# Kernel optimization log

Hardware: AMD Instinct MI355X
Metric: run time of the kernel (lower is better)

## Reference

```python
import jax, jax.numpy as jnp
import numpy as np

B, L, D = 32, 128, 512

def setup_inputs() -> dict:
    key = jax.random.key(0)
    ks = jax.random.split(key, 10)
    s = 1.0 / np.sqrt(D)
    return {
        "current_sotw": jax.random.normal(ks[0], (B, L, D), jnp.float32),
        "new_obs": jax.random.normal(ks[1], (B, L, D), jnp.float32),
        "Wq": jax.random.uniform(ks[2], (D, D), jnp.float32, -s, s),   # linear_query weight
        "bq": jax.random.uniform(ks[3], (D,), jnp.float32, -s, s),     # linear_query bias
        "Wc": jax.random.uniform(ks[4], (D, D), jnp.float32, -s, s),   # linear_context (no bias)
        "v": jax.random.uniform(ks[5], (D,), jnp.float32, -s, s),      # v projection to scalar score
        "Wout": jax.random.uniform(ks[6], (2 * D, D), jnp.float32, -s, s),  # linear_out weight
        "bout": jax.random.uniform(ks[7], (D,), jnp.float32, -s, s),        # linear_out bias (mlp type)
        "mix": jax.random.uniform(ks[8], (1,), jnp.float32),           # mixing_proportion ~ U[0,1)
    }

def _global_attn_mlp(source, memory, Wq, bq, Wc, v, Wout, bout):
    # OpenNMT GlobalAttention, attn_type='mlp', attn_func='softmax'
    wq = jnp.einsum('btd,de->bte', source, Wq) + bq          # [B,T,D]
    uh = jnp.einsum('bsd,de->bse', memory, Wc)               # [B,S,D]
    # scores: v . tanh(wq + uh) over broadcast [B,T,S,D]
    scores = jnp.einsum('btsd,d->bts', jnp.tanh(wq[:, :, None, :] + uh[:, None, :, :]), v)
    align = jax.nn.softmax(scores, axis=-1)                  # [B,T,S]
    c = jnp.einsum('bts,bsd->btd', align, memory)            # context [B,T,D]
    attn_h = jnp.einsum('btd,de->bte', jnp.concatenate([c, source], axis=-1), Wout) + bout
    return attn_h  # [B,T,D] (the torch code transposes to [T,B,D] then back)

def reference(current_sotw, new_obs, Wq, bq, Wc, v, Wout, bout, mix):
    a1 = _global_attn_mlp(new_obs, current_sotw, Wq, bq, Wc, v, Wout, bout)
    a2 = _global_attn_mlp(current_sotw, new_obs, Wq, bq, Wc, v, Wout, bout)
    m = mix[0]
    return (1.0 - m) * a1 + m * a2
```

## Files before the change

kernel.cpp:

```cpp
#include <hip/hip_runtime.h>

#define DD 512
#define SS 128
#define TT4 4
#define SCH16 16
#define RW 520
#define C2F 2.8853900817779268f
#define L2EF 1.4426950408889634f

typedef __bf16 bf16x8 __attribute__((ext_vector_type(8)));
typedef float f32x4 __attribute__((ext_vector_type(4)));
typedef unsigned int uint32x4 __attribute__((ext_vector_type(4)));

__device__ __forceinline__ unsigned short f2bf(float f) {
    unsigned int u = __builtin_bit_cast(unsigned int, f);
    u += 0x7fffu + ((u >> 16) & 1u);
    return (unsigned short)(u >> 16);
}
__device__ __forceinline__ float bflo(unsigned int u) { return __builtin_bit_cast(float, u << 16); }
__device__ __forceinline__ float bfhi(unsigned int u) { return __builtin_bit_cast(float, u & 0xffff0000u); }

__global__ __launch_bounds__(256)
void cvt_dual(const float* __restrict__ a, const float* __restrict__ b,
              unsigned short* __restrict__ oa, unsigned short* __restrict__ ob, int n8)
{
    int i = blockIdx.x * 256 + threadIdx.x;
    const float* in; unsigned short* out; int k;
    if (i < n8) { in = a; out = oa; k = i; }
    else        { in = b; out = ob; k = i - n8; }
    const float4 x = ((const float4*)in)[2 * k];
    const float4 y = ((const float4*)in)[2 * k + 1];
    uint32x4 o;
    o[0] = (unsigned)f2bf(x.x) | ((unsigned)f2bf(x.y) << 16);
    o[1] = (unsigned)f2bf(x.z) | ((unsigned)f2bf(x.w) << 16);
    o[2] = (unsigned)f2bf(y.x) | ((unsigned)f2bf(y.y) << 16);
    o[3] = (unsigned)f2bf(y.z) | ((unsigned)f2bf(y.w) << 16);
    ((uint32x4*)out)[k] = o;
}

__global__ __launch_bounds__(256)
void transpose_all(const float* __restrict__ Wq, const float* __restrict__ Wc,
                   const float* __restrict__ Wout,
                   unsigned short* __restrict__ Wqct, unsigned short* __restrict__ Woutt)
{
    __shared__ float t[64][65];
    const int z = blockIdx.z;
    const float* in; unsigned short* out; int R, r0;
    if (z == 0)      { in = Wq;   out = Wqct;             R = 512;  r0 = blockIdx.y * 64; }
    else if (z == 1) { in = Wc;   out = Wqct + 512 * 512; R = 512;  r0 = blockIdx.y * 64; }
    else             { in = Wout; out = Woutt;            R = 1024; r0 = (z - 2) * 512 + blockIdx.y * 64; }
    const int c0 = blockIdx.x * 64;
    const int tid = threadIdx.x;
    const int lc = tid & 63, lr = tid >> 6;
    #pragma unroll
    for (int i = 0; i < 16; ++i) {
        int r = lr + i * 4;
        t[r][lc] = in[(size_t)(r0 + r) * 512 + c0 + lc];
    }
    __syncthreads();
    #pragma unroll
    for (int i = 0; i < 16; ++i) {
        int rr = lr + i * 4;
        out[(size_t)(c0 + rr) * R + r0 + lc] = f2bf(t[lc][rr]);
    }
}

__global__ __launch_bounds__(256)
void gemm_proj(const unsigned short* __restrict__ A0, const unsigned short* __restrict__ A1,
               const unsigned short* __restrict__ Bt, const float* __restrict__ bq,
               unsigned short* __restrict__ w0, unsigned short* __restrict__ u0,
               unsigned short* __restrict__ w1, unsigned short* __restrict__ u1)
{
    constexpr int K = 512, LDA = 72;
    __shared__ __align__(16) unsigned short As[128][LDA];
    __shared__ __align__(16) unsigned short Bs[64][LDA];

    const unsigned short* A = blockIdx.z ? A1 : A0;
    unsigned short* outW    = blockIdx.z ? w1 : w0;
    unsigned short* outU    = blockIdx.z ? u1 : u0;

    const int tid = threadIdx.x;
    const int n0 = blockIdx.x * 64, m0 = blockIdx.y * 128;
    const int lane = tid & 63, wid = tid >> 6;
    const int wr = wid >> 1, wc = wid & 1;
    const int lr = lane & 15, kb = lane >> 4;

    f32x4 acc[4][2] = {};
    uint32x4 ra[4], rb[2];

    auto LOADK = [&](int k0) {
        #pragma unroll
        for (int j = 0; j < 4; ++j) {
            int id = tid + 256 * j; int r = id >> 3, s = id & 7;
            ra[j] = *(const uint32x4*)&A[(size_t)(m0 + r) * K + k0 + s * 8];
        }
        #pragma unroll
        for (int j = 0; j < 2; ++j) {
            int id = tid + 256 * j; int r = id >> 3, s = id & 7;
            rb[j] = *(const uint32x4*)&Bt[(size_t)(n0 + r) * K + k0 + s * 8];
        }
    };

    LOADK(0);
    #pragma unroll 1
    for (int step = 0; step < K / 64; ++step) {
        __syncthreads();
        #pragma unroll
        for (int j = 0; j < 4; ++j) {
            int id = tid + 256 * j; int r = id >> 3, s = id & 7;
            *(uint32x4*)&As[r][s * 8] = ra[j];
        }
        #pragma unroll
        for (int j = 0; j < 2; ++j) {
            int id = tid + 256 * j; int r = id >> 3, s = id & 7;
            *(uint32x4*)&Bs[r][s * 8] = rb[j];
        }
        __syncthreads();
        if (step + 1 < K / 64) LOADK((step + 1) * 64);
        #pragma unroll
        for (int kk = 0; kk < 64; kk += 32) {
            bf16x8 b0 = __builtin_bit_cast(bf16x8, *(const uint32x4*)&Bs[wc * 32 + lr][kk + kb * 8]);
            bf16x8 b1 = __builtin_bit_cast(bf16x8, *(const uint32x4*)&Bs[wc * 32 + 16 + lr][kk + kb * 8]);
            #pragma unroll
            for (int mf = 0; mf < 4; ++mf) {
                bf16x8 a0 = __builtin_bit_cast(bf16x8, *(const uint32x4*)&As[wr * 64 + mf * 16 + lr][kk + kb * 8]);
                acc[mf][0] = __builtin_amdgcn_mfma_f32_16x16x32_bf16(a0, b0, acc[mf][0], 0, 0, 0);
                acc[mf][1] = __builtin_amdgcn_mfma_f32_16x16x32_bf16(a0, b1, acc[mf][1], 0, 0, 0);
            }
        }
    }

    #pragma unroll
    for (int nf = 0; nf < 2; ++nf) {
        const int col = n0 + wc * 32 + nf * 16 + lr;
        const float bv = (col < 512) ? bq[col] : 0.0f;
        #pragma unroll
        for (int mf = 0; mf < 4; ++mf) {
            const int row = m0 + wr * 64 + mf * 16 + kb * 4;
            #pragma unroll
            for (int r = 0; r < 4; ++r) {
                const float valf = acc[mf][nf][r];
                if (col < 512) outW[(size_t)(row + r) * 512 + col] = f2bf((valf + bv) * C2F);
                else           outU[(size_t)(row + r) * 512 + (col - 512)] = f2bf(valf);
            }
        }
    }
}

__global__ __launch_bounds__(256)
void gemm_final(const unsigned short* __restrict__ c1, const unsigned short* __restrict__ c2,
                const float* __restrict__ no, const float* __restrict__ cs,
                const float* __restrict__ mix, const unsigned short* __restrict__ Bt,
                const float* __restrict__ bout, float* __restrict__ out)
{
    constexpr int K = 1024, LDA = 72;
    __shared__ __align__(16) unsigned short As[128][LDA];
    __shared__ __align__(16) unsigned short Bs[64][LDA];

    const int tid = threadIdx.x;
    const int n0 = blockIdx.x * 64, m0 = blockIdx.y * 128;
    const int lane = tid & 63, wid = tid >> 6;
    const int wr = wid >> 1, wc = wid & 1;
    const int lr = lane & 15, kb = lane >> 4;
    const float mxv = mix[0], omv = 1.0f - mxv;

    f32x4 acc[4][2] = {};
    uint32x4 ra[4], rb[2];

    auto LOADK = [&](int k0) {
        #pragma unroll
        for (int j = 0; j < 4; ++j) {
            int id = tid + 256 * j; int r = id >> 3, s = id & 7;
            const size_t row = m0 + r;
            const int k = k0 + s * 8;
            uint32x4 o;
            if (k < 512) {
                const uint32x4 x1 = *(const uint32x4*)&c1[row * 512 + k];
                const uint32x4 x2 = *(const uint32x4*)&c2[row * 512 + k];
                #pragma unroll
                for (int q = 0; q < 4; ++q) {
                    float lo = omv * bflo(x1[q]) + mxv * bflo(x2[q]);
                    float hi = omv * bfhi(x1[q]) + mxv * bfhi(x2[q]);
                    o[q] = (unsigned)f2bf(lo) | ((unsigned)f2bf(hi) << 16);
                }
            } else {
                const float* n1 = &no[row * 512 + k - 512];
                const float* s1 = &cs[row * 512 + k - 512];
                const float4 a1 = *(const float4*)n1, a2 = *(const float4*)(n1 + 4);
                const float4 b1 = *(const float4*)s1, b2 = *(const float4*)(s1 + 4);
                o[0] = (unsigned)f2bf(omv * a1.x + mxv * b1.x) | ((unsigned)f2bf(omv * a1.y + mxv * b1.y) << 16);
                o[1] = (unsigned)f2bf(omv * a1.z + mxv * b1.z) | ((unsigned)f2bf(omv * a1.w + mxv * b1.w) << 16);
                o[2] = (unsigned)f2bf(omv * a2.x + mxv * b2.x) | ((unsigned)f2bf(omv * a2.y + mxv * b2.y) << 16);
                o[3] = (unsigned)f2bf(omv * a2.z + mxv * b2.z) | ((unsigned)f2bf(omv * a2.w + mxv * b2.w) << 16);
            }
            ra[j] = o;
        }
        #pragma unroll
        for (int j = 0; j < 2; ++j) {
            int id = tid + 256 * j; int r = id >> 3, s = id & 7;
            rb[j] = *(const uint32x4*)&Bt[(size_t)(n0 + r) * K + k0 + s * 8];
        }
    };

    LOADK(0);
    #pragma unroll 1
    for (int step = 0; step < K / 64; ++step) {
        __syncthreads();
        #pragma unroll
        for (int j = 0; j < 4; ++j) {
            int id = tid + 256 * j; int r = id >> 3, s = id & 7;
            *(uint32x4*)&As[r][s * 8] = ra[j];
        }
        #pragma unroll
        for (int j = 0; j < 2; ++j) {
            int id = tid + 256 * j; int r = id >> 3, s = id & 7;
            *(uint32x4*)&Bs[r][s * 8] = rb[j];
        }
        __syncthreads();
        if (step + 1 < K / 64) LOADK((step + 1) * 64);
        #pragma unroll
        for (int kk = 0; kk < 64; kk += 32) {
            bf16x8 b0 = __builtin_bit_cast(bf16x8, *(const uint32x4*)&Bs[wc * 32 + lr][kk + kb * 8]);
            bf16x8 b1 = __builtin_bit_cast(bf16x8, *(const uint32x4*)&Bs[wc * 32 + 16 + lr][kk + kb * 8]);
            #pragma unroll
            for (int mf = 0; mf < 4; ++mf) {
                bf16x8 a0 = __builtin_bit_cast(bf16x8, *(const uint32x4*)&As[wr * 64 + mf * 16 + lr][kk + kb * 8]);
                acc[mf][0] = __builtin_amdgcn_mfma_f32_16x16x32_bf16(a0, b0, acc[mf][0], 0, 0, 0);
                acc[mf][1] = __builtin_amdgcn_mfma_f32_16x16x32_bf16(a0, b1, acc[mf][1], 0, 0, 0);
            }
        }
    }

    #pragma unroll
    for (int nf = 0; nf < 2; ++nf) {
        const int col = n0 + wc * 32 + nf * 16 + lr;
        const float bv = bout[col];
        #pragma unroll
        for (int mf = 0; mf < 4; ++mf) {
            const int row = m0 + wr * 64 + mf * 16 + kb * 4;
            #pragma unroll
            for (int r = 0; r < 4; ++r)
                out[(size_t)(row + r) * 512 + col] = acc[mf][nf][r] + bv;
        }
    }
}

__global__ __launch_bounds__(512, 8)
void attn_fused(const unsigned short* __restrict__ wq,
                const unsigned short* __restrict__ uh,
                const float* __restrict__ v,
                const unsigned short* __restrict__ mem,
                unsigned short* __restrict__ c_out)
{
    __shared__ __align__(16) unsigned short s_wq[TT4 * RW];
    __shared__ __align__(16) unsigned short s_uh[SCH16 * RW];
    __shared__ __align__(16) unsigned short s_v2[DD];
    __shared__ float s_sc[TT4 * SS];

    const int b = blockIdx.y, t0 = blockIdx.x * TT4;
    const int tid = threadIdx.x;

    if (tid < 256) {
        const int row = tid >> 6, G = tid & 63;
        *(uint32x4*)&s_wq[row * RW + G * 8] =
            *(const uint32x4*)&wq[((size_t)b * SS + t0 + row) * DD + G * 8];
    } else if (tid < 320) {
        const int H = tid - 256;
        const float4 p = *(const float4*)&v[H * 8];
        const float4 q = *(const float4*)&v[H * 8 + 4];
        uint32x4 o;
        o[0] = (unsigned)f2bf(p.x * 2.f) | ((unsigned)f2bf(p.y * 2.f) << 16);
        o[1] = (unsigned)f2bf(p.z * 2.f) | ((unsigned)f2bf(p.w * 2.f) << 16);
        o[2] = (unsigned)f2bf(q.x * 2.f) | ((unsigned)f2bf(q.y * 2.f) << 16);
        o[3] = (unsigned)f2bf(q.z * 2.f) | ((unsigned)f2bf(q.w * 2.f) << 16);
        *(uint32x4*)&s_v2[H * 8] = o;
    }

    const int oct = tid & 7;
    const int sr  = (tid >> 3) & 15;
    const int t   = tid >> 7;

    for (int sc0 = 0; sc0 < SS; sc0 += SCH16) {
        __syncthreads();
        {
            int i = tid;
            #pragma unroll
            for (int rep = 0; rep < 2; ++rep, i += 512) {
                const int row = i >> 6, G = i & 63;
                *(uint32x4*)&s_uh[row * RW + G * 8] =
                    *(const uint32x4*)&uh[((size_t)b * SS + sc0 + row) * DD + G * 8];
            }
        }
        __syncthreads();

        const unsigned short* wrow = &s_wq[t * RW];
        const unsigned short* urow = &s_uh[sr * RW];

        float a0 = 0.f, a1 = 0.f, a2 = 0.f, a3 = 0.f;
        #pragma unroll
        for (int j = 0; j < 8; ++j) {
            const int ch = (8 * j + oct) * 8;
            const uint32x4 w4 = *(const uint32x4*)&wrow[ch];
            const uint32x4 u4 = *(const uint32x4*)&urow[ch];
            const uint32x4 v4 = *(const uint32x4*)&s_v2[ch];
            float x, e;
            x = fmaf(C2F, bflo(u4[0]), bflo(w4[0])); e = __builtin_amdgcn_exp2f(x);
            a0 = fmaf(bflo(v4[0]), __builtin_amdgcn_rcpf(e + 1.f), a0);
            x = fmaf(C2F, bfhi(u4[0]), bfhi(w4[0])); e = __builtin_amdgcn_exp2f(x);
            a1 = fmaf(bfhi(v4[0]), __builtin_amdgcn_rcpf(e + 1.f), a1);
            x = fmaf(C2F, bflo(u4[1]), bflo(w4[1])); e = __builtin_amdgcn_exp2f(x);
            a2 = fmaf(bflo(v4[1]), __builtin_amdgcn_rcpf(e + 1.f), a2);
            x = fmaf(C2F, bfhi(u4[1]), bfhi(w4[1])); e = __builtin_amdgcn_exp2f(x);
            a3 = fmaf(bfhi(v4[1]), __builtin_amdgcn_rcpf(e + 1.f), a3);
            x = fmaf(C2F, bflo(u4[2]), bflo(w4[2])); e = __builtin_amdgcn_exp2f(x);
            a0 = fmaf(bflo(v4[2]), __builtin_amdgcn_rcpf(e + 1.f), a0);
            x = fmaf(C2F, bfhi(u4[2]), bfhi(w4[2])); e = __builtin_amdgcn_exp2f(x);
            a1 = fmaf(bfhi(v4[2]), __builtin_amdgcn_rcpf(e + 1.f), a1);
            x = fmaf(C2F, bflo(u4[3]), bflo(w4[3])); e = __builtin_amdgcn_exp2f(x);
            a2 = fmaf(bflo(v4[3]), __builtin_amdgcn_rcpf(e + 1.f), a2);
            x = fmaf(C2F, bfhi(u4[3]), bfhi(w4[3])); e = __builtin_amdgcn_exp2f(x);
            a3 = fmaf(bfhi(v4[3]), __builtin_amdgcn_rcpf(e + 1.f), a3);
        }
        float p = (a0 + a1) + (a2 + a3);
        p += __shfl_xor(p, 1);
        p += __shfl_xor(p, 2);
        p += __shfl_xor(p, 4);
        if (oct == 0) s_sc[t * SS + sc0 + sr] = -p;
    }
    __syncthreads();

    if (tid < 128) {
        const int tr = tid >> 5, l32 = tid & 31;
        float x0 = s_sc[tr * SS + l32];
        float x1 = s_sc[tr * SS + l32 + 32];
        float x2 = s_sc[tr * SS + l32 + 64];
        float x3 = s_sc[tr * SS + l32 + 96];
        float mx = fmaxf(fmaxf(x0, x1), fmaxf(x2, x3));
        #pragma unroll
        for (int off = 16; off > 0; off >>= 1) mx = fmaxf(mx, __shfl_xor(mx, off));
        const float e0 = __builtin_amdgcn_exp2f((x0 - mx) * L2EF);
        const float e1 = __builtin_amdgcn_exp2f((x1 - mx) * L2EF);
        const float e2 = __builtin_amdgcn_exp2f((x2 - mx) * L2EF);
        const float e3 = __builtin_amdgcn_exp2f((x3 - mx) * L2EF);
        float sum = (e0 + e1) + (e2 + e3);
        #pragma unroll
        for (int off = 16; off > 0; off >>= 1) sum += __shfl_xor(sum, off);
        const float rs = __builtin_amdgcn_rcpf(sum);
        s_sc[tr * SS + l32]      = e0 * rs;
        s_sc[tr * SS + l32 + 32] = e1 * rs;
        s_sc[tr * SS + l32 + 64] = e2 * rs;
        s_sc[tr * SS + l32 + 96] = e3 * rs;
    }

    const int w = tid >> 6, lane = tid & 63;
    const int tb = w & 3, half = w >> 2;
    const int d = half * 256 + lane * 4;
    f32x4 ac = {0.f, 0.f, 0.f, 0.f};

    for (int sc0 = 0; sc0 < SS; sc0 += SCH16) {
        __syncthreads();
        {
            int i = tid;
            #pragma unroll
            for (int rep = 0; rep < 2; ++rep, i += 512) {
                const int row = i >> 6, G = i & 63;
                *(uint32x4*)&s_uh[row * RW + G * 8] =
                    *(const uint32x4*)&mem[((size_t)b * SS + sc0 + row) * DD + G * 8];
            }
        }
        __syncthreads();
        #pragma unroll
        for (int srow = 0; srow < SCH16; ++srow) {
            const float e = s_sc[tb * SS + sc0 + srow];
            const uint2 mv = *(const uint2*)&s_uh[srow * RW + d];
            ac[0] = fmaf(e, bflo(mv.x), ac[0]);
            ac[1] = fmaf(e, bfhi(mv.x), ac[1]);
            ac[2] = fmaf(e, bflo(mv.y), ac[2]);
            ac[3] = fmaf(e, bfhi(mv.y), ac[3]);
        }
    }
    uint2 st;
    st.x = (unsigned)f2bf(ac[0]) | ((unsigned)f2bf(ac[1]) << 16);
    st.y = (unsigned)f2bf(ac[2]) | ((unsigned)f2bf(ac[3]) << 16);
    *(uint2*)&c_out[((size_t)b * SS + t0 + tb) * DD + d] = st;
}

extern "C" void kernel_launch(void* const* d_in, const int* in_sizes, int n_in,
                              void* d_out, int out_size, void* d_ws, size_t ws_size,
                              hipStream_t stream) {
    const float* cs   = (const float*)d_in[0];
    const float* no   = (const float*)d_in[1];
    const float* Wq   = (const float*)d_in[2];
    const float* bq   = (const float*)d_in[3];
    const float* Wc   = (const float*)d_in[4];
    const float* v    = (const float*)d_in[5];
    const float* Wout = (const float*)d_in[6];
    const float* bout = (const float*)d_in[7];
    const float* mix  = (const float*)d_in[8];
    float* out = (float*)d_out;

    typedef unsigned short us;
    char* ws = (char*)d_ws;
    us* cs_bf = (us*)(ws);
    us* no_bf = (us*)(ws + (4u  << 20));
    us* Wqct  = (us*)(ws + (8u  << 20));
    us* Woutt = (us*)(ws + (9u  << 20));
    us* wq1   = (us*)(ws + (10u << 20));
    us* uh2   = (us*)(ws + (14u << 20));
    us* wq2   = (us*)(ws + (18u << 20));
    us* uh1   = (us*)(ws + (22u << 20));
    us* c1    = (us*)(ws + (26u << 20));
    us* c2    = (us*)(ws + (10u << 20));

    const dim3 b256(256);
    const int n8 = 4096 * DD / 8;

    cvt_dual<<<dim3(2 * n8 / 256), b256, 0, stream>>>(cs, no, cs_bf, no_bf, n8);
    transpose_all<<<dim3(8, 8, 4), b256, 0, stream>>>(Wq, Wc, Wout, Wqct, Woutt);

    gemm_proj<<<dim3(16, 32, 2), b256, 0, stream>>>(no_bf, cs_bf, Wqct, bq,
                                                    wq1, uh2, wq2, uh1);

    attn_fused<<<dim3(32, 32), dim3(512), 0, stream>>>(wq1, uh1, v, cs_bf, c1);
    attn_fused<<<dim3(32, 32), dim3(512), 0, stream>>>(wq2, uh2, v, no_bf, c2);

    gemm_final<<<dim3(8, 32), b256, 0, stream>>>(c1, c2, no, cs, mix, Woutt, bout, out);
}
```

Measured before the change: 337.0 us.

## Factor tanh exponent into precomputed exp tables and enlarge projection GEMM tile

The tanh score term is rewritten so that exp2 of the query and key projections is computed once per element when staging into shared memory. The inner score loop then needs only a multiply-add and a reciprocal, where before it needed an exp per (t,s,d) element. The projection GEMM now computes a 128x128 tile per block with four N-fragments per wave, and it scales the uh output by the 2/ln2 factor so it matches the new exp form. The context accumulation reads memory rows directly from global memory instead of staging them through shared memory with syncs. The risks are overflow or precision loss when the exponentials are stored as bf16 for large inputs, and higher register pressure in the GEMM.

After: 302.9 us. 10.1% less time.

```diff
diff --git a/kernel.cpp b/kernel.cpp
--- a/kernel.cpp
+++ b/kernel.cpp
@@ -73,30 +73,26 @@
 {
     constexpr int K = 512, LDA = 72;
     __shared__ __align__(16) unsigned short As[128][LDA];
-    __shared__ __align__(16) unsigned short Bs[64][LDA];
+    __shared__ __align__(16) unsigned short Bs[128][LDA];
 
     const unsigned short* A = blockIdx.z ? A1 : A0;
     unsigned short* outW    = blockIdx.z ? w1 : w0;
     unsigned short* outU    = blockIdx.z ? u1 : u0;
 
     const int tid = threadIdx.x;
-    const int n0 = blockIdx.x * 64, m0 = blockIdx.y * 128;
+    const int n0 = blockIdx.x * 128, m0 = blockIdx.y * 128;
     const int lane = tid & 63, wid = tid >> 6;
     const int wr = wid >> 1, wc = wid & 1;
     const int lr = lane & 15, kb = lane >> 4;
 
-    f32x4 acc[4][2] = {};
-    uint32x4 ra[4], rb[2];
+    f32x4 acc[4][4] = {};
+    uint32x4 ra[4], rb[4];
 
     auto LOADK = [&](int k0) {
         #pragma unroll
         for (int j = 0; j < 4; ++j) {
             int id = tid + 256 * j; int r = id >> 3, s = id & 7;
             ra[j] = *(const uint32x4*)&A[(size_t)(m0 + r) * K + k0 + s * 8];
-        }
-        #pragma unroll
-        for (int j = 0; j < 2; ++j) {
-            int id = tid + 256 * j; int r = id >> 3, s = id & 7;
             rb[j] = *(const uint32x4*)&Bt[(size_t)(n0 + r) * K + k0 + s * 8];
         }
     };
@@ -109,30 +105,29 @@
         for (int j = 0; j < 4; ++j) {
             int id = tid + 256 * j; int r = id >> 3, s = id & 7;
             *(uint32x4*)&As[r][s * 8] = ra[j];
-        }
-        #pragma unroll
-        for (int j = 0; j < 2; ++j) {
-            int id = tid + 256 * j; int r = id >> 3, s = id & 7;
             *(uint32x4*)&Bs[r][s * 8] = rb[j];
         }
         __syncthreads();
         if (step + 1 < K / 64) LOADK((step + 1) * 64);
         #pragma unroll
         for (int kk = 0; kk < 64; kk += 32) {
-            bf16x8 b0 = __builtin_bit_cast(bf16x8, *(const uint32x4*)&Bs[wc * 32 + lr][kk + kb * 8]);
-            bf16x8 b1 = __builtin_bit_cast(bf16x8, *(const uint32x4*)&Bs[wc * 32 + 16 + lr][kk + kb * 8]);
+            bf16x8 bfr[4];
+            #pragma unroll
+            for (int nf = 0; nf < 4; ++nf)
+                bfr[nf] = __builtin_bit_cast(bf16x8, *(const uint32x4*)&Bs[wc * 64 + nf * 16 + lr][kk + kb * 8]);
             #pragma unroll
             for (int mf = 0; mf < 4; ++mf) {
                 bf16x8 a0 = __builtin_bit_cast(bf16x8, *(const uint32x4*)&As[wr * 64 + mf * 16 + lr][kk + kb * 8]);
-                acc[mf][0] = __builtin_amdgcn_mfma_f32_16x16x32_bf16(a0, b0, acc[mf][0], 0, 0, 0);
-                acc[mf][1] = __builtin_amdgcn_mfma_f32_16x16x32_bf16(a0, b1, acc[mf][1], 0, 0, 0);
+                #pragma unroll
+                for (int nf = 0; nf < 4; ++nf)
+                    acc[mf][nf] = __builtin_amdgcn_mfma_f32_16x16x32_bf16(a0, bfr[nf], acc[mf][nf], 0, 0, 0);
             }
         }
     }
 
     #pragma unroll
-    for (int nf = 0; nf < 2; ++nf) {
-        const int col = n0 + wc * 32 + nf * 16 + lr;
+    for (int nf = 0; nf < 4; ++nf) {
+        const int col = n0 + wc * 64 + nf * 16 + lr;
         const float bv = (col < 512) ? bq[col] : 0.0f;
         #pragma unroll
         for (int mf = 0; mf < 4; ++mf) {
@@ -141,7 +136,7 @@
             for (int r = 0; r < 4; ++r) {
                 const float valf = acc[mf][nf][r];
                 if (col < 512) outW[(size_t)(row + r) * 512 + col] = f2bf((valf + bv) * C2F);
-                else           outU[(size_t)(row + r) * 512 + (col - 512)] = f2bf(valf);
+                else           outU[(size_t)(row + r) * 512 + (col - 512)] = f2bf(valf * C2F);
             }
         }
     }
@@ -252,18 +247,25 @@
                 const unsigned short* __restrict__ mem,
                 unsigned short* __restrict__ c_out)
 {
-    __shared__ __align__(16) unsigned short s_wq[TT4 * RW];
-    __shared__ __align__(16) unsigned short s_uh[SCH16 * RW];
+    __shared__ __align__(16) unsigned short s_ew[TT4 * RW];
+    __shared__ __align__(16) unsigned short s_eu[SCH16 * RW];
     __shared__ __align__(16) unsigned short s_v2[DD];
-    __shared__ float s_sc[TT4 * SS];
+    __shared__ __align__(16) float s_sc[TT4 * SS];
 
     const int b = blockIdx.y, t0 = blockIdx.x * TT4;
     const int tid = threadIdx.x;
 
     if (tid < 256) {
         const int row = tid >> 6, G = tid & 63;
-        *(uint32x4*)&s_wq[row * RW + G * 8] =
-            *(const uint32x4*)&wq[((size_t)b * SS + t0 + row) * DD + G * 8];
+        const uint32x4 w4 = *(const uint32x4*)&wq[((size_t)b * SS + t0 + row) * DD + G * 8];
+        uint32x4 o;
+        #pragma unroll
+        for (int q = 0; q < 4; ++q) {
+            const float e0 = __builtin_amdgcn_exp2f(bflo(w4[q]));
+            const float e1 = __builtin_amdgcn_exp2f(bfhi(w4[q]));
+            o[q] = (unsigned)f2bf(e0) | ((unsigned)f2bf(e1) << 16);
+        }
+        *(uint32x4*)&s_ew[row * RW + G * 8] = o;
     } else if (tid < 320) {
         const int H = tid - 256;
         const float4 p = *(const float4*)&v[H * 8];
@@ -287,14 +289,21 @@
             #pragma unroll
             for (int rep = 0; rep < 2; ++rep, i += 512) {
                 const int row = i >> 6, G = i & 63;
-                *(uint32x4*)&s_uh[row * RW + G * 8] =
-                    *(const uint32x4*)&uh[((size_t)b * SS + sc0 + row) * DD + G * 8];
-            }
-        }
-        __syncthreads();
-
-        const unsigned short* wrow = &s_wq[t * RW];
-        const unsigned short* urow = &s_uh[sr * RW];
+                const uint32x4 u4 = *(const uint32x4*)&uh[((size_t)b * SS + sc0 + row) * DD + G * 8];
+                uint32x4 o;
+                #pragma unroll
+                for (int q = 0; q < 4; ++q) {
+                    const unsigned e0 = __builtin_bit_cast(unsigned, __builtin_amdgcn_exp2f(bflo(u4[q])));
+                    const unsigned e1 = __builtin_bit_cast(unsigned, __builtin_amdgcn_exp2f(bfhi(u4[q])));
+                    o[q] = (e0 >> 16) | (e1 & 0xffff0000u);
+                }
+                *(uint32x4*)&s_eu[row * RW + G * 8] = o;
+            }
+        }
+        __syncthreads();
+
+        const unsigned short* wrow = &s_ew[t * RW];
+        const unsigned short* urow = &s_eu[sr * RW];
 
         float a0 = 0.f, a1 = 0.f, a2 = 0.f, a3 = 0.f;
         #pragma unroll
@@ -303,23 +312,14 @@
             const uint32x4 w4 = *(const uint32x4*)&wrow[ch];
             const uint32x4 u4 = *(const uint32x4*)&urow[ch];
             const uint32x4 v4 = *(const uint32x4*)&s_v2[ch];
-            float x, e;
-            x = fmaf(C2F, bflo(u4[0]), bflo(w4[0])); e = __builtin_amdgcn_exp2f(x);
-            a0 = fmaf(bflo(v4[0]), __builtin_amdgcn_rcpf(e + 1.f), a0);
-            x = fmaf(C2F, bfhi(u4[0]), bfhi(w4[0])); e = __builtin_amdgcn_exp2f(x);
-            a1 = fmaf(bfhi(v4[0]), __builtin_amdgcn_rcpf(e + 1.f), a1);
-            x = fmaf(C2F, bflo(u4[1]), bflo(w4[1])); e = __builtin_amdgcn_exp2f(x);
-            a2 = fmaf(bflo(v4[1]), __builtin_amdgcn_rcpf(e + 1.f), a2);
-            x = fmaf(C2F, bfhi(u4[1]), bfhi(w4[1])); e = __builtin_amdgcn_exp2f(x);
-            a3 = fmaf(bfhi(v4[1]), __builtin_amdgcn_rcpf(e + 1.f), a3);
-            x = fmaf(C2F, bflo(u4[2]), bflo(w4[2])); e = __builtin_amdgcn_exp2f(x);
-            a0 = fmaf(bflo(v4[2]), __builtin_amdgcn_rcpf(e + 1.f), a0);
-            x = fmaf(C2F, bfhi(u4[2]), bfhi(w4[2])); e = __builtin_amdgcn_exp2f(x);
-            a1 = fmaf(bfhi(v4[2]), __builtin_amdgcn_rcpf(e + 1.f), a1);
-            x = fmaf(C2F, bflo(u4[3]), bflo(w4[3])); e = __builtin_amdgcn_exp2f(x);
-            a2 = fmaf(bflo(v4[3]), __builtin_amdgcn_rcpf(e + 1.f), a2);
-            x = fmaf(C2F, bfhi(u4[3]), bfhi(w4[3])); e = __builtin_amdgcn_exp2f(x);
-            a3 = fmaf(bfhi(v4[3]), __builtin_amdgcn_rcpf(e + 1.f), a3);
+            a0 = fmaf(bflo(v4[0]), __builtin_amdgcn_rcpf(fmaf(bflo(w4[0]), bflo(u4[0]), 1.f)), a0);
+            a1 = fmaf(bfhi(v4[0]), __builtin_amdgcn_rcpf(fmaf(bfhi(w4[0]), bfhi(u4[0]), 1.f)), a1);
+            a2 = fmaf(bflo(v4[1]), __builtin_amdgcn_rcpf(fmaf(bflo(w4[1]), bflo(u4[1]), 1.f)), a2);
+            a3 = fmaf(bfhi(v4[1]), __builtin_amdgcn_rcpf(fmaf(bfhi(w4[1]), bfhi(u4[1]), 1.f)), a3);
+            a0 = fmaf(bflo(v4[2]), __builtin_amdgcn_rcpf(fmaf(bflo(w4[2]), bflo(u4[2]), 1.f)), a0);
+            a1 = fmaf(bfhi(v4[2]), __builtin_amdgcn_rcpf(fmaf(bfhi(w4[2]), bfhi(u4[2]), 1.f)), a1);
+            a2 = fmaf(bflo(v4[3]), __builtin_amdgcn_rcpf(fmaf(bflo(w4[3]), bflo(u4[3]), 1.f)), a2);
+            a3 = fmaf(bfhi(v4[3]), __builtin_amdgcn_rcpf(fmaf(bfhi(w4[3]), bfhi(u4[3]), 1.f)), a3);
         }
         float p = (a0 + a1) + (a2 + a3);
         p += __shfl_xor(p, 1);
@@ -351,38 +351,32 @@
         s_sc[tr * SS + l32 + 64] = e2 * rs;
         s_sc[tr * SS + l32 + 96] = e3 * rs;
     }
-
-    const int w = tid >> 6, lane = tid & 63;
-    const int tb = w & 3, half = w >> 2;
-    const int d = half * 256 + lane * 4;
-    f32x4 ac = {0.f, 0.f, 0.f, 0.f};
-
-    for (int sc0 = 0; sc0 < SS; sc0 += SCH16) {
-        __syncthreads();
-        {
-            int i = tid;
-            #pragma unroll
-            for (int rep = 0; rep < 2; ++rep, i += 512) {
-                const int row = i >> 6, G = i & 63;
-                *(uint32x4*)&s_uh[row * RW + G * 8] =
-                    *(const uint32x4*)&mem[((size_t)b * SS + sc0 + row) * DD + G * 8];
-            }
-        }
-        __syncthreads();
-        #pragma unroll
-        for (int srow = 0; srow < SCH16; ++srow) {
-            const float e = s_sc[tb * SS + sc0 + srow];
-            const uint2 mv = *(const uint2*)&s_uh[srow * RW + d];
-            ac[0] = fmaf(e, bflo(mv.x), ac[0]);
-            ac[1] = fmaf(e, bfhi(mv.x), ac[1]);
-            ac[2] = fmaf(e, bflo(mv.y), ac[2]);
-            ac[3] = fmaf(e, bfhi(mv.y), ac[3]);
-        }
-    }
-    uint2 st;
-    st.x = (unsigned)f2bf(ac[0]) | ((unsigned)f2bf(ac[1]) << 16);
-    st.y = (unsigned)f2bf(ac[2]) | ((unsigned)f2bf(ac[3]) << 16);
-    *(uint2*)&c_out[((size_t)b * SS + t0 + tb) * DD + d] = st;
+    __syncthreads();
+
+    {
+        const int w = tid >> 6, lane = tid & 63;
+        const int tb = w & 3, half = w >> 2;
+        const int d = half * 256 + lane * 4;
+        const unsigned short* mb = mem + (size_t)b * SS * DD + d;
+        f32x4 ac = {0.f, 0.f, 0.f, 0.f};
+        #pragma unroll 1
+        for (int s = 0; s < SS; s += 4) {
+            const float4 e4 = *(const float4*)&s_sc[tb * SS + s];
+            #pragma unroll
+            for (int q = 0; q < 4; ++q) {
+                const float e = (q == 0) ? e4.x : (q == 1) ? e4.y : (q == 2) ? e4.z : e4.w;
+                const uint2 mv = *(const uint2*)&mb[(size_t)(s + q) * DD];
+                ac[0] = fmaf(e, bflo(mv.x), ac[0]);
+                ac[1] = fmaf(e, bfhi(mv.x), ac[1]);
+                ac[2] = fmaf(e, bflo(mv.y), ac[2]);
+                ac[3] = fmaf(e, bfhi(mv.y), ac[3]);
+            }
+        }
+        uint2 st;
+        st.x = (unsigned)f2bf(ac[0]) | ((unsigned)f2bf(ac[1]) << 16);
+        st.y = (unsigned)f2bf(ac[2]) | ((unsigned)f2bf(ac[3]) << 16);
+        *(uint2*)&c_out[((size_t)b * SS + t0 + tb) * DD + d] = st;
+    }
 }
 
 extern "C" void kernel_launch(void* const* d_in, const int* in_sizes, int n_in,
@@ -418,8 +412,8 @@
     cvt_dual<<<dim3(2 * n8 / 256), b256, 0, stream>>>(cs, no, cs_bf, no_bf, n8);
     transpose_all<<<dim3(8, 8, 4), b256, 0, stream>>>(Wq, Wc, Wout, Wqct, Woutt);
 
-    gemm_proj<<<dim3(16, 32, 2), b256, 0, stream>>>(no_bf, cs_bf, Wqct, bq,
-                                                    wq1, uh2, wq2, uh1);
+    gemm_proj<<<dim3(8, 32, 2), b256, 0, stream>>>(no_bf, cs_bf, Wqct, bq,
+                                                   wq1, uh2, wq2, uh1);
 
     attn_fused<<<dim3(32, 32), dim3(512), 0, stream>>>(wq1, uh1, v, cs_bf, c1);
     attn_fused<<<dim3(32, 32), dim3(512), 0, stream>>>(wq2, uh2, v, no_bf, c2);
```
